# Kernel optimization log

Measured on AMD Instinct MI355X. Metric: run time of the kernel, lower is better.

## Reference

```python
import jax, jax.numpy as jnp
import numpy as np

N, E, IN, H, OUT, L = 20000, 320000, 256, 256, 128, 3
EPS = 1e-5


def setup_inputs() -> dict:
    key = jax.random.key(0)
    ks = jax.random.split(key, 16)
    s = 0.02
    return {
        "x": jax.random.normal(ks[0], (N, IN), jnp.float32),
        "edge_index": jax.random.randint(ks[1], (2, E), 0, N, jnp.int64),
        "in_w": jax.random.normal(ks[2], (IN, H), jnp.float32) * s,
        "in_b": jnp.zeros((H,), jnp.float32),
        "parent_w": jax.random.normal(ks[3], (L, H, H), jnp.float32) * s,
        "child_w": jax.random.normal(ks[4], (L, H, H), jnp.float32) * s,
        "self_w": jax.random.normal(ks[5], (L, H, H), jnp.float32) * s,
        "self_b": jnp.zeros((L, H), jnp.float32),
        "ln_g": jnp.ones((L, H), jnp.float32),
        "ln_b": jnp.zeros((L, H), jnp.float32),
        "head_w1": jax.random.normal(ks[6], (H, H), jnp.float32) * s,
        "head_b1": jnp.zeros((H,), jnp.float32),
        "head_w2": jax.random.normal(ks[7], (H, OUT), jnp.float32) * s,
        "head_b2": jnp.zeros((OUT,), jnp.float32),
    }


def _aggregate(h, src, dst, weight):
    # gather -> matmul -> scatter-add -> degree-normalize
    transformed = h[src] @ weight                       # [E, H]
    agg = jax.ops.segment_sum(transformed, dst, num_segments=N)
    deg = jax.ops.segment_sum(jnp.ones((src.shape[0],), h.dtype), dst, num_segments=N)
    deg = jnp.maximum(deg, 1.0)
    return agg / deg[:, None]


def _layer_norm(x, g, b):
    mu = jnp.mean(x, axis=-1, keepdims=True)
    var = jnp.mean(jnp.square(x - mu), axis=-1, keepdims=True)
    return (x - mu) * jax.lax.rsqrt(var + EPS) * g + b


def reference(x, edge_index, in_w, in_b, parent_w, child_w, self_w, self_b,
              ln_g, ln_b, head_w1, head_b1, head_w2, head_b2):
    src, dst = edge_index[0], edge_index[1]
    h = x @ in_w + in_b                                  # input_proj
    for l in range(L):
        parent_msg = _aggregate(h, src, dst, parent_w[l])
        child_msg = _aggregate(h, dst, src, child_w[l])  # reversed edges
        out = h @ self_w[l] + self_b[l] + parent_msg + child_msg
        out = jax.nn.gelu(out, approximate=False)
        # dropout is identity in eval mode (training=False)
        h = _layer_norm(h + out, ln_g[l], ln_b[l])
    y = jax.nn.gelu(h @ head_w1 + head_b1, approximate=False)
    return y @ head_w2 + head_b2
```

## Files before the change

kernel.cpp:

```cpp
#include <hip/hip_runtime.h>


#define H 256
#define LAYERS 3
#define OUTD 128
#define LN_EPS 1e-5f

typedef short s16x8 __attribute__((ext_vector_type(8)));
typedef unsigned short u16x4 __attribute__((ext_vector_type(4)));
typedef unsigned short u16x8 __attribute__((ext_vector_type(8)));
typedef float f32x4 __attribute__((ext_vector_type(4)));
typedef int i32x4 __attribute__((ext_vector_type(4)));

__device__ __forceinline__ unsigned short f2bf(float f) {
  unsigned int u = __float_as_uint(f);
  u += 0x7FFFu + ((u >> 16) & 1u);
  return (unsigned short)(u >> 16);
}
__device__ __forceinline__ float bf2f(unsigned short s) {
  return __uint_as_float(((unsigned int)s) << 16);
}
__device__ __forceinline__ float gelu_f(float x) {
  return 0.5f * x * (1.0f + erff(x * 0.70710678118654752440f));
}
__device__ __forceinline__ void gload16(const void* g, void* l) {
  __builtin_amdgcn_global_load_lds((const __attribute__((address_space(1))) void*)g,
                                   (__attribute__((address_space(3))) void*)l, 16, 0, 0);
}


__device__ __forceinline__ void store_split8(unsigned short* __restrict__ T, int NS, int sec,
                                             int row, int l, u16x4 hv, u16x4 lv) {
  size_t tb = ((size_t)((row >> 4) * NS + sec) << 4) + (l >> 3);
  int off = (((row & 15) + (((l >> 1) & 3) << 4)) << 3) + ((l & 1) << 2);
  *(u16x4*)(T + tb * 512 + off) = hv;
  *(u16x4*)(T + (tb + 8) * 512 + off) = lv;
}

__global__ void split_tiles_kernel(const float* __restrict__ X,
                                   unsigned short* __restrict__ T, int NS,
                                   unsigned short* __restrict__ Hc, int M)
{
  const int rb = blockIdx.x;
  const int l = threadIdx.x & 63;
  const int cq = threadIdx.x >> 6;
  const int row = (rb << 4) + (l & 15);
  if (row >= M) return;
  const float* xr = X + (size_t)row * H;
#pragma unroll
  for (int p = 0; p < 2; ++p) {
    const int c = cq + (p << 2);
    const int j0 = (c << 5) + ((l >> 4) << 3);
    f32x4 v0 = *(const f32x4*)(xr + j0);
    f32x4 v1 = *(const f32x4*)(xr + j0 + 4);
    u16x8 hv, lv;
#pragma unroll
    for (int i = 0; i < 4; ++i) {
      unsigned short hb = f2bf(v0[i]); hv[i] = hb;     lv[i] = f2bf(v0[i] - bf2f(hb));
      unsigned short hc = f2bf(v1[i]); hv[4 + i] = hc; lv[4 + i] = f2bf(v1[i] - bf2f(hc));
    }
    size_t tb = ((size_t)(rb * NS) << 4);
    *(u16x8*)(T + (tb + c) * 512 + (l << 3)) = hv;
    *(u16x8*)(T + (tb + c + 8) * 512 + (l << 3)) = lv;
    if (Hc) *(u16x8*)(Hc + (size_t)row * H + j0) = hv;
  }
}

__global__ void bext_all_kernel(const float* __restrict__ in_w,
                                const float* __restrict__ parent_w,
                                const float* __restrict__ child_w,
                                const float* __restrict__ self_w,
                                const float* __restrict__ head_w1,
                                const float* __restrict__ head_w2,
                                unsigned short* __restrict__ Bext)
{
  const int slot = blockIdx.x >> 8;
  const int chunk = blockIdx.x & 255;
  const int ncol = (slot == 11) ? OUTD : H;
  const int idx = chunk * 256 + threadIdx.x;
  if (idx >= H * ncol) return;
  const float* W =
    (slot == 0)  ? in_w :
    (slot <= 3)  ? parent_w + (size_t)(slot - 1) * H * H :
    (slot <= 6)  ? child_w  + (size_t)(slot - 4) * H * H :
    (slot <= 9)  ? self_w   + (size_t)(slot - 7) * H * H :
    (slot == 10) ? head_w1  : head_w2;
  unsigned short* Bt = Bext + (size_t)slot * H * 512;
  int k = idx / ncol;
  int n = idx - k * ncol;
  float w = W[idx];
  unsigned short hb = f2bf(w);
  unsigned short lb = f2bf(w - bf2f(hb));
  size_t base = (((size_t)(n >> 4) << 4) + (k >> 5)) * 512 +
                (((n & 15) + (((k >> 3) & 3) << 4)) << 3) + (k & 7);
  Bt[base] = hb;
  Bt[base + 8 * 512] = lb;
}

__global__ void zero2_kernel(int* __restrict__ a, int* __restrict__ b, int n) {
  int i = blockIdx.x * 256 + threadIdx.x;
  if (i < n) { a[i] = 0; b[i] = 0; }
}

__global__ void deg_kernel(const int* __restrict__ src, const int* __restrict__ dst,
                           int* __restrict__ di, int* __restrict__ dox, int E) {
  int e = blockIdx.x * 256 + threadIdx.x;
  if (e >= E) return;
  atomicAdd(&dox[src[e]], 1);
  atomicAdd(&di[dst[e]], 1);
}

__global__ void rdeg_kernel(const int* __restrict__ di, const int* __restrict__ dox,
                            float* __restrict__ ri, float* __restrict__ ro,
                            int* __restrict__ cur_in, int* __restrict__ cur_out, int n) {
  int i = blockIdx.x * 256 + threadIdx.x;
  if (i >= n) return;
  int a = di[i];  if (a < 1) a = 1;
  int b = dox[i]; if (b < 1) b = 1;
  ri[i] = 1.0f / (float)a;
  ro[i] = 1.0f / (float)b;
  cur_in[i] = 0;
  cur_out[i] = 0;
}

__global__ __launch_bounds__(1024)
void scan2_kernel(const int* __restrict__ degi, const int* __restrict__ dego,
                  int* __restrict__ rp_in, int* __restrict__ rp_out, int n) {
  __shared__ int partial[1024];
  const int* deg = blockIdx.x ? dego : degi;
  int* rowptr = blockIdx.x ? rp_out : rp_in;
  const int t = threadIdx.x;
  const int chunk = (n + 1023) / 1024;
  int b = t * chunk;
  int e = b + chunk; if (e > n) e = n;
  int s = 0;
  for (int i = b; i < e; ++i) s += deg[i];
  partial[t] = s;
  __syncthreads();
  for (int off = 1; off < 1024; off <<= 1) {
    int v = (t >= off) ? partial[t - off] : 0;
    __syncthreads();
    partial[t] += v;
    __syncthreads();
  }
  int run = (t == 0) ? 0 : partial[t - 1];
  for (int i = b; i < e; ++i) { rowptr[i] = run; run += deg[i]; }
  if (t == 1023) rowptr[n] = run;
}

__global__ void fill_kernel(const int* __restrict__ src, const int* __restrict__ dst,
                            const int* __restrict__ rp_in, const int* __restrict__ rp_out,
                            int* __restrict__ cur_in, int* __restrict__ cur_out,
                            int* __restrict__ ci_in, int* __restrict__ ci_out, int E) {
  int e = blockIdx.x * 256 + threadIdx.x;
  if (e >= E) return;
  int s = src[e], d = dst[e];
  int p = atomicAdd(&cur_in[d], 1);
  ci_in[rp_in[d] + p] = s;
  int q = atomicAdd(&cur_out[s], 1);
  ci_out[rp_out[s] + q] = d;
}

template<int NF, int GELU, int SPLIT>
__global__ __launch_bounds__(256)
void gemm_kernel(const unsigned short* __restrict__ A, int NSa,
                 const unsigned short* __restrict__ B0,
                 const unsigned short* __restrict__ B1,
                 const unsigned short* __restrict__ B2,
                 const float* __restrict__ bias, float* __restrict__ C,
                 unsigned short* __restrict__ Asp, int NSp,
                 unsigned short* __restrict__ Hc,
                 int M, int nrb, int nsec)
{
  constexpr int N = NF * 64;
  __shared__ unsigned short ldsA[2][2048];

  const int tid = threadIdx.x;
  const int lane = tid & 63;
  const int wn = tid >> 6;
  const int m0 = blockIdx.x << 5;
  int rbw = (blockIdx.x << 1) + (wn & 1);
  if (rbw >= nrb) rbw = nrb - 1;
  const int hilo = wn >> 1;

  f32x4 acc[2][NF] = {};

  auto STAGE = [&](int buf, int step) {
    const int s = step >> 3;
    const int c = step & 7;
    const unsigned short* pa =
        A + (((size_t)(rbw * NSa + s) << 4) + c + (hilo << 3)) * 512 + (lane << 3);
    gload16(pa, &ldsA[buf][0] + (wn << 9));
  };

  auto COMPUTE = [&](int buf, int step) {
    const int s = step >> 3;
    const int c = step & 7;
    const unsigned short* Bs = (s == 0) ? B0 : ((s == 1) ? B1 : B2);
    s16x8 bh[NF], bl[NF];
#pragma unroll
    for (int j = 0; j < NF; ++j) {
      const int g = wn * NF + j;
      bh[j] = *(const s16x8*)(Bs + ((size_t)((g << 4) + c) << 9) + (lane << 3));
      bl[j] = *(const s16x8*)(Bs + ((size_t)((g << 4) + c + 8) << 9) + (lane << 3));
    }
    const unsigned short* base = &ldsA[buf][0];
    s16x8 ah[2], al[2];
#pragma unroll
    for (int f = 0; f < 2; ++f) {
      ah[f] = *(const s16x8*)(base + (f << 9) + (lane << 3));
      al[f] = *(const s16x8*)(base + 1024 + (f << 9) + (lane << 3));
    }
#pragma unroll
    for (int i = 0; i < 2; ++i)
#pragma unroll
      for (int j = 0; j < NF; ++j)
        acc[i][j] = __builtin_amdgcn_mfma_f32_16x16x32_bf16(ah[i], bh[j], acc[i][j], 0, 0, 0);
#pragma unroll
    for (int i = 0; i < 2; ++i)
#pragma unroll
      for (int j = 0; j < NF; ++j)
        acc[i][j] = __builtin_amdgcn_mfma_f32_16x16x32_bf16(ah[i], bl[j], acc[i][j], 0, 0, 0);
#pragma unroll
    for (int i = 0; i < 2; ++i)
#pragma unroll
      for (int j = 0; j < NF; ++j)
        acc[i][j] = __builtin_amdgcn_mfma_f32_16x16x32_bf16(al[i], bh[j], acc[i][j], 0, 0, 0);
  };

  const int nsteps = nsec << 3;
  STAGE(0, 0);
  int cur = 0;
  for (int t = 0; t < nsteps - 1; ++t) {
    STAGE(cur ^ 1, t + 1);
    asm volatile("s_waitcnt vmcnt(1)" ::: "memory");
    __builtin_amdgcn_s_barrier();
    COMPUTE(cur, t);
    asm volatile("s_waitcnt lgkmcnt(0)" ::: "memory");
    __builtin_amdgcn_s_barrier();
    cur ^= 1;
  }
  asm volatile("s_waitcnt vmcnt(0)" ::: "memory");
  __builtin_amdgcn_s_barrier();
  COMPUTE(cur, nsteps - 1);

  const int r0 = (lane >> 4) << 2;
  const int cn = lane & 15;
#pragma unroll
  for (int j = 0; j < NF; ++j) {
    const int col = wn * (NF << 4) + (j << 4) + cn;
    const float bb = bias ? bias[col] : 0.0f;
#pragma unroll
    for (int i = 0; i < 2; ++i) {
      const int rowb = m0 + (i << 4) + r0;
#pragma unroll
      for (int r = 0; r < 4; ++r) {
        const int rr = rowb + r;
        if (rr < M) {
          float v = acc[i][j][r] + bb;
          if (GELU) v = gelu_f(v);
          if (C) C[(size_t)rr * N + col] = v;
          if (SPLIT) {
            unsigned short hb = f2bf(v);
            size_t tb = (((size_t)(rr >> 4) * NSp) << 4) + (col >> 5);
            int off = ((rr & 15) << 3) + (((col >> 3) & 3) << 7) + (col & 7);
            Asp[tb * 512 + off] = hb;
            Asp[(tb + 8) * 512 + off] = f2bf(v - bf2f(hb));
            if (Hc) Hc[((size_t)rr << 8) + col] = hb;
          }
        }
      }
    }
  }
}

__device__ __forceinline__ void gacc8(const int* __restrict__ ci, int beg, int end,
                                      const unsigned short* __restrict__ Hc, int foff,
                                      float* __restrict__ acc) {
  int i = beg;
  for (; i < end && (i & 3); ++i) {
    u16x8 a = *(const u16x8*)(Hc + ((size_t)ci[i] << 8) + foff);
#pragma unroll
    for (int z = 0; z < 8; ++z) acc[z] += bf2f(a[z]);
  }
  for (; i + 4 <= end; i += 4) {
    i32x4 id = *(const i32x4*)(ci + i);
    u16x8 a = *(const u16x8*)(Hc + ((size_t)id[0] << 8) + foff);
    u16x8 b = *(const u16x8*)(Hc + ((size_t)id[1] << 8) + foff);
    u16x8 c = *(const u16x8*)(Hc + ((size_t)id[2] << 8) + foff);
    u16x8 d = *(const u16x8*)(Hc + ((size_t)id[3] << 8) + foff);
#pragma unroll
    for (int z = 0; z < 8; ++z)
      acc[z] += (bf2f(a[z]) + bf2f(b[z])) + (bf2f(c[z]) + bf2f(d[z]));
  }
  for (; i < end; ++i) {
    u16x8 a = *(const u16x8*)(Hc + ((size_t)ci[i] << 8) + foff);
#pragma unroll
    for (int z = 0; z < 8; ++z) acc[z] += bf2f(a[z]);
  }
}

__global__ __launch_bounds__(128)
void gather_kernel(
    const int* __restrict__ rp_in, const int* __restrict__ ci_in,
    const int* __restrict__ rp_out, const int* __restrict__ ci_out,
    const float* __restrict__ ri, const float* __restrict__ ro,
    const unsigned short* __restrict__ Hc, unsigned short* __restrict__ Aext,
    int M, int nrb)
{
  __shared__ unsigned short sh[2][2][2][512];
  const int b = blockIdx.x;
  const int xcd = b & 7;
  const int s = xcd >> 1;
  const int rb = ((b >> 3) << 1) + (xcd & 1);
  if (rb >= nrb) return;
  const int tid = threadIdx.x;
  const int g = tid >> 3;
  const int t = tid & 7;
  const int row = (rb << 4) + g;
  const int foff = (s << 6) + (t << 3);

  float hin[8] = {}, hout[8] = {};
  float wi = 0.f, wo = 0.f;
  if (row < M) {
    gacc8(ci_in,  rp_in[row],  rp_in[row + 1],  Hc, foff, hin);
    gacc8(ci_out, rp_out[row], rp_out[row + 1], Hc, foff, hout);
    wi = ri[row];
    wo = ro[row];
  }

  const int cc = t >> 2;
  const int pos = (g << 3) + ((t & 3) << 7);
  u16x8 hv, lv;
#pragma unroll
  for (int q = 0; q < 8; ++q) {
    float v = hin[q] * wi;
    unsigned short hb = f2bf(v);
    hv[q] = hb; lv[q] = f2bf(v - bf2f(hb));
  }
  *(u16x8*)(&sh[0][0][cc][pos]) = hv;
  *(u16x8*)(&sh[0][1][cc][pos]) = lv;
#pragma unroll
  for (int q = 0; q < 8; ++q) {
    float v = hout[q] * wo;
    unsigned short hb = f2bf(v);
    hv[q] = hb; lv[q] = f2bf(v - bf2f(hb));
  }
  *(u16x8*)(&sh[1][0][cc][pos]) = hv;
  *(u16x8*)(&sh[1][1][cc][pos]) = lv;
  __syncthreads();

  const int tp = tid >> 4;
  const int q = tid & 15;
  const int sec = tp >> 2, hilo = (tp >> 1) & 1, c2 = tp & 1;
  const int cg = (s << 1) + c2 + (hilo << 3);
  size_t tile = ((size_t)(rb * 3 + 1 + sec) << 4) + cg;
  unsigned short* dstp = Aext + tile * 512;
  const unsigned short* srcp = &sh[sec][hilo][c2][0];
#pragma unroll
  for (int i = 0; i < 4; ++i)
    *(u16x8*)(dstp + (i << 7) + (q << 3)) = *(const u16x8*)(srcp + (i << 7) + (q << 3));
}

__global__ void finalize_kernel(float* __restrict__ h, const float* __restrict__ P,
                                unsigned short* __restrict__ Aext,
                                unsigned short* __restrict__ Hc,
                                const float* __restrict__ g, const float* __restrict__ b, int M)
{
  int row = blockIdx.x * 4 + (threadIdx.x >> 6);
  if (row >= M) return;
  int l = threadIdx.x & 63;
  int j = l << 2;
  f32x4 hv = *(const f32x4*)(h + (size_t)row * H + j);
  f32x4 pv = *(const f32x4*)(P + (size_t)row * H + j);
  f32x4 t;
  float sum = 0.f, sq = 0.f;
#pragma unroll
  for (int i = 0; i < 4; ++i) {
    t[i] = hv[i] + gelu_f(pv[i]);
    sum += t[i];
    sq += t[i] * t[i];
  }
#pragma unroll
  for (int off = 1; off < 64; off <<= 1) {
    sum += __shfl_xor(sum, off, 64);
    sq  += __shfl_xor(sq, off, 64);
  }
  float mu = sum * (1.0f / H);
  float var = sq * (1.0f / H) - mu * mu;
  float rs = rsqrtf(var + LN_EPS);
  f32x4 outv;
  u16x4 hvv, lvv;
#pragma unroll
  for (int i = 0; i < 4; ++i) {
    outv[i] = (t[i] - mu) * rs * g[j + i] + b[j + i];
    unsigned short hb = f2bf(outv[i]);
    hvv[i] = hb;
    lvv[i] = f2bf(outv[i] - bf2f(hb));
  }
  *(f32x4*)(h + (size_t)row * H + j) = outv;
  *(u16x4*)(Hc + ((size_t)row << 8) + j) = hvv;
  store_split8(Aext, 3, 0, row, l, hvv, lvv);
}

extern "C" void kernel_launch(void* const* d_in, const int* in_sizes, int n_in,
                              void* d_out, int out_size, void* d_ws, size_t ws_size,
                              hipStream_t stream)
{
  const float* x        = (const float*)d_in[0];
  const int*   ei       = (const int*)d_in[1];
  const float* in_w     = (const float*)d_in[2];
  const float* in_b     = (const float*)d_in[3];
  const float* parent_w = (const float*)d_in[4];
  const float* child_w  = (const float*)d_in[5];
  const float* self_w   = (const float*)d_in[6];
  const float* self_b   = (const float*)d_in[7];
  const float* ln_g     = (const float*)d_in[8];
  const float* ln_b     = (const float*)d_in[9];
  const float* head_w1  = (const float*)d_in[10];
  const float* head_b1  = (const float*)d_in[11];
  const float* head_w2  = (const float*)d_in[12];
  const float* head_b2  = (const float*)d_in[13];

  const int M = in_sizes[0] / H;
  const int E = in_sizes[1] / 2;
  const int nrb = (M + 15) / 16;
  const int* src = ei;
  const int* dst = ei + E;

  char* w = (char*)d_ws;
  auto alloc = [&](size_t bytes) { char* p = w; w += (bytes + 255) & ~(size_t)255; return p; };
  float*          h    = (float*)alloc((size_t)M * H * 4);
  float*          P    = (float*)alloc((size_t)M * H * 4);
  unsigned short* Ax   = (unsigned short*)alloc((size_t)nrb * 16 * 512 * 2);
  unsigned short* Aext = (unsigned short*)alloc((size_t)nrb * 48 * 512 * 2);
  unsigned short* Hc   = (unsigned short*)alloc((size_t)M * H * 2);
  unsigned short* Bext = (unsigned short*)alloc((size_t)12 * H * 512 * 2);
  int*            degi = (int*)alloc((size_t)M * 4);
  int*            dego = (int*)alloc((size_t)M * 4);
  float*          ri   = (float*)alloc((size_t)M * 4);
  float*          ro   = (float*)alloc((size_t)M * 4);
  int*            rp_in   = (int*)alloc((size_t)(M + 1) * 4);
  int*            rp_out  = (int*)alloc((size_t)(M + 1) * 4);
  int*            cur_in  = (int*)alloc((size_t)M * 4);
  int*            cur_out = (int*)alloc((size_t)M * 4);
  int*            ci_in   = (int*)alloc((size_t)E * 4);
  int*            ci_out  = (int*)alloc((size_t)E * 4);
  if ((size_t)(w - (char*)d_ws) > ws_size) return;

  auto bslot = [&](int i) { return Bext + (size_t)i * H * 512; };

  bext_all_kernel<<<12 * 256, 256, 0, stream>>>(in_w, parent_w, child_w, self_w,
                                                head_w1, head_w2, Bext);

  zero2_kernel<<<(M + 255) / 256, 256, 0, stream>>>(degi, dego, M);
  deg_kernel<<<(E + 255) / 256, 256, 0, stream>>>(src, dst, degi, dego, E);
  rdeg_kernel<<<(M + 255) / 256, 256, 0, stream>>>(degi, dego, ri, ro, cur_in, cur_out, M);
  scan2_kernel<<<2, 1024, 0, stream>>>(degi, dego, rp_in, rp_out, M);
  fill_kernel<<<(E + 255) / 256, 256, 0, stream>>>(src, dst, rp_in, rp_out,
                                                   cur_in, cur_out, ci_in, ci_out, E);

  const int mb32 = (M + 31) / 32;
  const int ggrid = (M + 3) / 4;
  const int xgrid = 8 * ((nrb + 1) / 2);

  split_tiles_kernel<<<nrb, 256, 0, stream>>>(x, Ax, 1, nullptr, M);
  gemm_kernel<4, 0, 1><<<mb32, 256, 0, stream>>>(Ax, 1, bslot(0), nullptr, nullptr,
                                                 in_b, h, Aext, 3, Hc, M, nrb, 1);

  for (int l = 0; l < LAYERS; ++l) {
    gather_kernel<<<xgrid, 128, 0, stream>>>(rp_in, ci_in, rp_out, ci_out,
                                             ri, ro, Hc, Aext, M, nrb);
    gemm_kernel<4, 0, 0><<<mb32, 256, 0, stream>>>(Aext, 3,
                                                   bslot(7 + l), bslot(1 + l), bslot(4 + l),
                                                   self_b + (size_t)l * H, P,
                                                   nullptr, 0, nullptr, M, nrb, 3);
    finalize_kernel<<<ggrid, 256, 0, stream>>>(h, P, Aext, Hc,
                                               ln_g + (size_t)l * H, ln_b + (size_t)l * H, M);
  }

  gemm_kernel<4, 1, 1><<<mb32, 256, 0, stream>>>(Aext, 3, bslot(10), nullptr, nullptr,
                                                 head_b1, nullptr, Ax, 1, nullptr, M, nrb, 1);
  gemm_kernel<2, 0, 0><<<mb32, 256, 0, stream>>>(Ax, 1, bslot(11), nullptr, nullptr,
                                                 head_b2, (float*)d_out, nullptr, 0, nullptr,
                                                 M, nrb, 1);
}
```

Measured before the change: 441.5 us.

## Drop low-bf16 split for aggregated messages and unroll gather by eight

The gather kernel now stores only the high bf16 part of the degree-normalized neighbour sums instead of a hi/lo pair. This halves its LDS staging and global writes. The layer GEMM gets a TWOTERM mode that runs its aggregated-message sections over 8 k-steps instead of 16, pairing two 32-wide chunks per step with one A tile each. This cuts both A traffic and MFMA count for those sections. The gather loop also gains an 8-wide unrolled path to keep more neighbour loads in flight, at the cost of lower precision in the message terms.

```diff
diff --git a/kernel.cpp b/kernel.cpp
--- a/kernel.cpp
+++ b/kernel.cpp
@@ -161,7 +161,7 @@
   ci_out[rp_out[s] + q] = d;
 }
 
-template<int NF, int GELU, int SPLIT>
+template<int NF, int GELU, int SPLIT, int TWOTERM>
 __global__ __launch_bounds__(256)
 void gemm_kernel(const unsigned short* __restrict__ A, int NSa,
                  const unsigned short* __restrict__ B0,
@@ -186,49 +186,86 @@
   f32x4 acc[2][NF] = {};
 
   auto STAGE = [&](int buf, int step) {
-    const int s = step >> 3;
-    const int c = step & 7;
+    int s, c;
+    if (!TWOTERM || step < 8) { s = step >> 3; c = (step & 7) + (hilo << 3); }
+    else { int t2 = step - 8; s = 1 + (t2 >> 2); c = ((t2 & 3) << 1) + hilo; }
     const unsigned short* pa =
-        A + (((size_t)(rbw * NSa + s) << 4) + c + (hilo << 3)) * 512 + (lane << 3);
+        A + (((size_t)(rbw * NSa + s) << 4) + c) * 512 + (lane << 3);
     gload16(pa, &ldsA[buf][0] + (wn << 9));
   };
 
   auto COMPUTE = [&](int buf, int step) {
-    const int s = step >> 3;
-    const int c = step & 7;
-    const unsigned short* Bs = (s == 0) ? B0 : ((s == 1) ? B1 : B2);
-    s16x8 bh[NF], bl[NF];
-#pragma unroll
-    for (int j = 0; j < NF; ++j) {
-      const int g = wn * NF + j;
-      bh[j] = *(const s16x8*)(Bs + ((size_t)((g << 4) + c) << 9) + (lane << 3));
-      bl[j] = *(const s16x8*)(Bs + ((size_t)((g << 4) + c + 8) << 9) + (lane << 3));
+    const unsigned short* base = &ldsA[buf][0];
+    s16x8 a0[2], a1[2];
+#pragma unroll
+    for (int f = 0; f < 2; ++f) {
+      a0[f] = *(const s16x8*)(base + (f << 9) + (lane << 3));
+      a1[f] = *(const s16x8*)(base + 1024 + (f << 9) + (lane << 3));
     }
-    const unsigned short* base = &ldsA[buf][0];
-    s16x8 ah[2], al[2];
-#pragma unroll
-    for (int f = 0; f < 2; ++f) {
-      ah[f] = *(const s16x8*)(base + (f << 9) + (lane << 3));
-      al[f] = *(const s16x8*)(base + 1024 + (f << 9) + (lane << 3));
+    if (!TWOTERM || step < 8) {
+      const int s = step >> 3;
+      const int c = step & 7;
+      const unsigned short* Bs = (s == 0) ? B0 : ((s == 1) ? B1 : B2);
+      s16x8 bh[NF], bl[NF];
+#pragma unroll
+      for (int j = 0; j < NF; ++j) {
+        const int g = wn * NF + j;
+        bh[j] = *(const s16x8*)(Bs + ((size_t)((g << 4) + c) << 9) + (lane << 3));
+        bl[j] = *(const s16x8*)(Bs + ((size_t)((g << 4) + c + 8) << 9) + (lane << 3));
+      }
+#pragma unroll
+      for (int i = 0; i < 2; ++i)
+#pragma unroll
+        for (int j = 0; j < NF; ++j)
+          acc[i][j] = __builtin_amdgcn_mfma_f32_16x16x32_bf16(a0[i], bh[j], acc[i][j], 0, 0, 0);
+#pragma unroll
+      for (int i = 0; i < 2; ++i)
+#pragma unroll
+        for (int j = 0; j < NF; ++j)
+          acc[i][j] = __builtin_amdgcn_mfma_f32_16x16x32_bf16(a0[i], bl[j], acc[i][j], 0, 0, 0);
+#pragma unroll
+      for (int i = 0; i < 2; ++i)
+#pragma unroll
+        for (int j = 0; j < NF; ++j)
+          acc[i][j] = __builtin_amdgcn_mfma_f32_16x16x32_bf16(a1[i], bh[j], acc[i][j], 0, 0, 0);
+    } else {
+      const int t2 = step - 8;
+      const int s = 1 + (t2 >> 2);
+      const int ca = (t2 & 3) << 1, cb = ca + 1;
+      const unsigned short* Bs = (s == 1) ? B1 : B2;
+      s16x8 bha[NF], bla[NF], bhb[NF], blb[NF];
+#pragma unroll
+      for (int j = 0; j < NF; ++j) {
+        const int g = wn * NF + j;
+        bha[j] = *(const s16x8*)(Bs + ((size_t)((g << 4) + ca) << 9) + (lane << 3));
+        bla[j] = *(const s16x8*)(Bs + ((size_t)((g << 4) + ca + 8) << 9) + (lane << 3));
+        bhb[j] = *(const s16x8*)(Bs + ((size_t)((g << 4) + cb) << 9) + (lane << 3));
+        blb[j] = *(const s16x8*)(Bs + ((size_t)((g << 4) + cb + 8) << 9) + (lane << 3));
+      }
+#pragma unroll
+      for (int i = 0; i < 2; ++i)
+#pragma unroll
+        for (int j = 0; j < NF; ++j)
+          acc[i][j] = __builtin_amdgcn_mfma_f32_16x16x32_bf16(a0[i], bha[j], acc[i][j], 0, 0, 0);
+#pragma unroll
+      for (int i = 0; i < 2; ++i)
+#pragma unroll
+        for (int j = 0; j < NF; ++j)
+          acc[i][j] = __builtin_amdgcn_mfma_f32_16x16x32_bf16(a0[i], bla[j], acc[i][j], 0, 0, 0);
+#pragma unroll
+      for (int i = 0; i < 2; ++i)
+#pragma unroll
+        for (int j = 0; j < NF; ++j)
+          acc[i][j] = __builtin_amdgcn_mfma_f32_16x16x32_bf16(a1[i], bhb[j], acc[i][j], 0, 0, 0);
+#pragma unroll
+      for (int i = 0; i < 2; ++i)
+#pragma unroll
+        for (int j = 0; j < NF; ++j)
+          acc[i][j] = __builtin_amdgcn_mfma_f32_16x16x32_bf16(a1[i], blb[j], acc[i][j], 0, 0, 0);
     }
-#pragma unroll
-    for (int i = 0; i < 2; ++i)
-#pragma unroll
-      for (int j = 0; j < NF; ++j)
-        acc[i][j] = __builtin_amdgcn_mfma_f32_16x16x32_bf16(ah[i], bh[j], acc[i][j], 0, 0, 0);
-#pragma unroll
-    for (int i = 0; i < 2; ++i)
-#pragma unroll
-      for (int j = 0; j < NF; ++j)
-        acc[i][j] = __builtin_amdgcn_mfma_f32_16x16x32_bf16(ah[i], bl[j], acc[i][j], 0, 0, 0);
-#pragma unroll
-    for (int i = 0; i < 2; ++i)
-#pragma unroll
-      for (int j = 0; j < NF; ++j)
-        acc[i][j] = __builtin_amdgcn_mfma_f32_16x16x32_bf16(al[i], bh[j], acc[i][j], 0, 0, 0);
   };
 
-  const int nsteps = nsec << 3;
+  const int nsteps = TWOTERM ? 16 : (nsec << 3);
   STAGE(0, 0);
   int cur = 0;
   for (int t = 0; t < nsteps - 1; ++t) {
@@ -283,6 +320,22 @@
 #pragma unroll
     for (int z = 0; z < 8; ++z) acc[z] += bf2f(a[z]);
   }
+  for (; i + 8 <= end; i += 8) {
+    i32x4 id0 = *(const i32x4*)(ci + i);
+    i32x4 id1 = *(const i32x4*)(ci + i + 4);
+    u16x8 a0 = *(const u16x8*)(Hc + ((size_t)id0[0] << 8) + foff);
+    u16x8 a1 = *(const u16x8*)(Hc + ((size_t)id0[1] << 8) + foff);
+    u16x8 a2 = *(const u16x8*)(Hc + ((size_t)id0[2] << 8) + foff);
+    u16x8 a3 = *(const u16x8*)(Hc + ((size_t)id0[3] << 8) + foff);
+    u16x8 a4 = *(const u16x8*)(Hc + ((size_t)id1[0] << 8) + foff);
+    u16x8 a5 = *(const u16x8*)(Hc + ((size_t)id1[1] << 8) + foff);
+    u16x8 a6 = *(const u16x8*)(Hc + ((size_t)id1[2] << 8) + foff);
+    u16x8 a7 = *(const u16x8*)(Hc + ((size_t)id1[3] << 8) + foff);
+#pragma unroll
+    for (int z = 0; z < 8; ++z)
+      acc[z] += ((bf2f(a0[z]) + bf2f(a1[z])) + (bf2f(a2[z]) + bf2f(a3[z]))) +
+                ((bf2f(a4[z]) + bf2f(a5[z])) + (bf2f(a6[z]) + bf2f(a7[z])));
+  }
   for (; i + 4 <= end; i += 4) {
     i32x4 id = *(const i32x4*)(ci + i);
     u16x8 a = *(const u16x8*)(Hc + ((size_t)id[0] << 8) + foff);
@@ -308,7 +361,7 @@
     const unsigned short* __restrict__ Hc, unsigned short* __restrict__ Aext,
     int M, int nrb)
 {
-  __shared__ unsigned short sh[2][2][2][512];
+  __shared__ unsigned short sh[2][2][512];
   const int b = blockIdx.x;
   const int xcd = b & 7;
   const int s = xcd >> 1;
@@ -331,35 +384,25 @@
 
   const int cc = t >> 2;
   const int pos = (g << 3) + ((t & 3) << 7);
-  u16x8 hv, lv;
-#pragma unroll
-  for (int q = 0; q < 8; ++q) {
-    float v = hin[q] * wi;
-    unsigned short hb = f2bf(v);
-    hv[q] = hb; lv[q] = f2bf(v - bf2f(hb));
-  }
-  *(u16x8*)(&sh[0][0][cc][pos]) = hv;
-  *(u16x8*)(&sh[0][1][cc][pos]) = lv;
-#pragma unroll
-  for (int q = 0; q < 8; ++q) {
-    float v = hout[q] * wo;
-    unsigned short hb = f2bf(v);
-    hv[q] = hb; lv[q] = f2bf(v - bf2f(hb));
-  }
-  *(u16x8*)(&sh[1][0][cc][pos]) = hv;
-  *(u16x8*)(&sh[1][1][cc][pos]) = lv;
+  u16x8 hv;
+#pragma unroll
+  for (int q = 0; q < 8; ++q) hv[q] = f2bf(hin[q] * wi);
+  *(u16x8*)(&sh[0][cc][pos]) = hv;
+#pragma unroll
+  for (int q = 0; q < 8; ++q) hv[q] = f2bf(hout[q] * wo);
+  *(u16x8*)(&sh[1][cc][pos]) = hv;
   __syncthreads();
 
-  const int tp = tid >> 4;
-  const int q = tid & 15;
-  const int sec = tp >> 2, hilo = (tp >> 1) & 1, c2 = tp & 1;
-  const int cg = (s << 1) + c2 + (hilo << 3);
+  const int tp = tid >> 5;
+  const int q = tid & 31;
+  const int sec = tp >> 1, c2 = tp & 1;
+  const int cg = (s << 1) + c2;
   size_t tile = ((size_t)(rb * 3 + 1 + sec) << 4) + cg;
   unsigned short* dstp = Aext + tile * 512;
-  const unsigned short* srcp = &sh[sec][hilo][c2][0];
-#pragma unroll
-  for (int i = 0; i < 4; ++i)
-    *(u16x8*)(dstp + (i << 7) + (q << 3)) = *(const u16x8*)(srcp + (i << 7) + (q << 3));
+  const unsigned short* srcp = &sh[sec][c2][0];
+#pragma unroll
+  for (int i = 0; i < 2; ++i)
+    *(u16x8*)(dstp + (i << 8) + (q << 3)) = *(const u16x8*)(srcp + (i << 8) + (q << 3));
 }
 
 __global__ void finalize_kernel(float* __restrict__ h, const float* __restrict__ P,
@@ -465,23 +508,23 @@
   const int xgrid = 8 * ((nrb + 1) / 2);
 
   split_tiles_kernel<<<nrb, 256, 0, stream>>>(x, Ax, 1, nullptr, M);
-  gemm_kernel<4, 0, 1><<<mb32, 256, 0, stream>>>(Ax, 1, bslot(0), nullptr, nullptr,
-                                                 in_b, h, Aext, 3, Hc, M, nrb, 1);
+  gemm_kernel<4, 0, 1, 0><<<mb32, 256, 0, stream>>>(Ax, 1, bslot(0), nullptr, nullptr,
+                                                    in_b, h, Aext, 3, Hc, M, nrb, 1);
 
   for (int l = 0; l < LAYERS; ++l) {
     gather_kernel<<<xgrid, 128, 0, stream>>>(rp_in, ci_in, rp_out, ci_out,
                                              ri, ro, Hc, Aext, M, nrb);
-    gemm_kernel<4, 0, 0><<<mb32, 256, 0, stream>>>(Aext, 3,
-                                                   bslot(7 + l), bslot(1 + l), bslot(4 + l),
-                                                   self_b + (size_t)l * H, P,
-                                                   nullptr, 0, nullptr, M, nrb, 3);
+    gemm_kernel<4, 0, 0, 1><<<mb32, 256, 0, stream>>>(Aext, 3,
+                                                      bslot(7 + l), bslot(1 + l), bslot(4 + l),
+                                                      self_b + (size_t)l * H, P,
+                                                      nullptr, 0, nullptr, M, nrb, 3);
     finalize_kernel<<<ggrid, 256, 0, stream>>>(h, P, Aext, Hc,
                                                ln_g + (size_t)l * H, ln_b + (size_t)l * H, M);
   }
 
-  gemm_kernel<4, 1, 1><<<mb32, 256, 0, stream>>>(Aext, 3, bslot(10), nullptr, nullptr,
-                                                 head_b1, nullptr, Ax, 1, nullptr, M, nrb, 1);
-  gemm_kernel<2, 0, 0><<<mb32, 256, 0, stream>>>(Ax, 1, bslot(11), nullptr, nullptr,
-                                                 head_b2, (float*)d_out, nullptr, 0, nullptr,
-                                                 M, nrb, 1);
-}
+  gemm_kernel<4, 1, 1, 0><<<mb32, 256, 0, stream>>>(Aext, 3, bslot(10), nullptr, nullptr,
+                                                    head_b1, nullptr, Ax, 1, nullptr, M, nrb, 1);
+  gemm_kernel<2, 0, 0, 0><<<mb32, 256, 0, stream>>>(Ax, 1, bslot(11), nullptr, nullptr,
+                                                    head_b2, (float*)d_out, nullptr, 0, nullptr,
+                                                    M, nrb, 1);
+}
```

Measured after the change: 565.7 us. +28.1%, slower.
